# Optimization experiments

Hardware: AMD Instinct MI355X
Metric: run time of the kernel (lower is better)

## Reference

```python
import jax, jax.numpy as jnp
import numpy as np

EPS = 1e-3  # keras LayerNormalization default epsilon

def layernorm(x, gamma, beta):
    mu = jnp.mean(x, axis=-1, keepdims=True)
    var = jnp.var(x, axis=-1, keepdims=True)
    return (x - mu) * jax.lax.rsqrt(var + EPS) * gamma + beta

def setup_inputs() -> dict:
    key = jax.random.key(0)
    ks = jax.random.split(key, 20)
    B, N, T, Dimg, H = 512, 100, 14, 2048, 768
    s = lambda k, *sh: jax.random.normal(k, sh, dtype=jnp.float32) * 0.02
    return {
        "img_feat": jax.random.normal(ks[0], (B, N, Dimg), dtype=jnp.float32),
        "ques_feat": jax.random.normal(ks[1], (B, T, H), dtype=jnp.float32),
        "Wc": s(ks[2], Dimg, H), "bc": jnp.zeros((H,), jnp.float32),
        "Wq": s(ks[3], H, H),    "bq": jnp.zeros((H,), jnp.float32),
        "Wi": s(ks[4], Dimg, H), "bi": jnp.zeros((H,), jnp.float32),
        "wqa": s(ks[5], H, 1), "bqa": jnp.zeros((1,), jnp.float32),
        "wia": s(ks[6], H, 1), "bia": jnp.zeros((1,), jnp.float32),
        "g1": jnp.ones((N,), jnp.float32), "b1": jnp.zeros((N,), jnp.float32),
        "g2": jnp.ones((H,), jnp.float32), "b2": jnp.zeros((H,), jnp.float32),
        "g3": jnp.ones((T,), jnp.float32), "b3": jnp.zeros((T,), jnp.float32),
        "g4": jnp.ones((H,), jnp.float32), "b4": jnp.zeros((H,), jnp.float32),
        "g5": jnp.ones((N,), jnp.float32), "b5": jnp.zeros((N,), jnp.float32),
    }

def reference(img_feat, ques_feat, Wc, bc, Wq, bq, Wi, bi, wqa, bqa, wia, bia,
              g1, b1, g2, b2, g3, b3, g4, b4, g5, b5):
    # img_feat: [B,N,Dimg], ques_feat: [B,T,H]
    img_corr = img_feat @ Wc + bc                                   # [B,N,H]
    wm = jnp.einsum('bth,bnh->btn', ques_feat, img_corr)            # [B,T,N]
    wm = jax.nn.relu(layernorm(wm, g1, b1))
    ques_embed = ques_feat @ Wq + bq                                # [B,T,H]
    img_embed = img_feat @ Wi + bi                                  # [B,N,H]
    transform_img = jnp.einsum('btn,bnh->bth', wm, img_embed)       # [B,T,H]
    ques_atten_sum = jax.nn.relu(layernorm(transform_img + ques_embed, g2, b2))
    # dropout is identity at inference
    ques_atten = (ques_atten_sum @ wqa + bqa)[..., 0]               # [B,T]
    ques_atten = jax.nn.softmax(layernorm(ques_atten, g3, b3), axis=-1)
    transform_ques = jnp.einsum('btn,bth->bnh', wm, ques_embed)     # [B,N,H]
    img_atten_sum = jax.nn.relu(layernorm(transform_ques + img_embed, g4, b4))
    img_atten = (img_atten_sum @ wia + bia)[..., 0]                 # [B,N]
    img_atten = jax.nn.softmax(layernorm(img_atten, g5, b5), axis=-1)
    ques_atten_feat = jnp.einsum('bt,bth->bh', ques_atten, ques_feat)  # [B,H]
    img_atten_feat = jnp.einsum('bn,bnd->bd', img_atten, img_feat)     # [B,Dimg]
    return (img_atten_feat, ques_atten_feat)
```

## Files before the change

### kernel.cpp

```cpp
#include <hip/hip_runtime.h>

using f32x4     = __attribute__((ext_vector_type(4))) float;
using bf16x8    = __attribute__((ext_vector_type(8))) short;
using ushort8_t = __attribute__((ext_vector_type(8))) unsigned short;

__device__ __forceinline__ unsigned short f2bf(float f) {
    unsigned u = __builtin_bit_cast(unsigned, f);
    u += 0x7fffu + ((u >> 16) & 1u);
    return (unsigned short)(u >> 16);
}
__device__ __forceinline__ float bf2f(unsigned short h) {
    return __builtin_bit_cast(float, (unsigned)h << 16);
}

__device__ __forceinline__ float wave_sum(float v) {
#pragma unroll
    for (int off = 32; off > 0; off >>= 1) v += __shfl_xor(v, off, 64);
    return v;
}
__device__ __forceinline__ float wave_max(float v) {
#pragma unroll
    for (int off = 32; off > 0; off >>= 1) v = fmaxf(v, __shfl_xor(v, off, 64));
    return v;
}

#define GLP(p)  ((const __attribute__((address_space(1))) void*)(p))
#define LDSP(p) ((__attribute__((address_space(3))) void*)(p))

__global__ __launch_bounds__(256) void cvt2(
    const float* __restrict__ in0, unsigned short* __restrict__ out0, long n80,
    const float* __restrict__ in1, unsigned short* __restrict__ out1, long n81, int split)
{
    const float* in; unsigned short* out; long n8, i, stride;
    if ((int)blockIdx.x < split) {
        in = in0; out = out0; n8 = n80;
        i = (long)blockIdx.x * 256 + threadIdx.x; stride = (long)split * 256;
    } else {
        in = in1; out = out1; n8 = n81;
        i = (long)(blockIdx.x - split) * 256 + threadIdx.x;
        stride = (long)(gridDim.x - split) * 256;
    }
    for (; i < n8; i += stride) {
        const float4* p = (const float4*)(in + i * 8);
        float4 a = p[0], b = p[1];
        ushort8_t v;
        v[0] = f2bf(a.x); v[1] = f2bf(a.y); v[2] = f2bf(a.z); v[3] = f2bf(a.w);
        v[4] = f2bf(b.x); v[5] = f2bf(b.y); v[6] = f2bf(b.z); v[7] = f2bf(b.w);
        *(ushort8_t*)(out + i * 8) = v;
    }
}

__global__ __launch_bounds__(256) void pack_t(
    const float* __restrict__ S0, const float* __restrict__ S1, int nsplit,
    unsigned short* __restrict__ D, int K)
{
    __shared__ float t[64][65];
    const int k0 = blockIdx.x * 64, n0 = blockIdx.y * 64;
    const float* S = (n0 < nsplit) ? S0 : S1;
    const int nb = (n0 < nsplit) ? n0 : n0 - nsplit;
    const int c = threadIdx.x & 63, r4 = threadIdx.x >> 6;
#pragma unroll
    for (int it = 0; it < 16; ++it) {
        int r = it * 4 + r4;
        t[r][c] = S[(size_t)(k0 + r) * nsplit + nb + c];
    }
    __syncthreads();
#pragma unroll
    for (int it = 0; it < 16; ++it) {
        int rn = it * 4 + r4;
        D[(size_t)(n0 + rn) * K + k0 + c] = f2bf(t[c][rn]);
    }
}

__global__ __launch_bounds__(512, 1) void gemm8(
    const unsigned short* __restrict__ A1, const unsigned short* __restrict__ Bt1,
    const float* __restrict__ b1a, const float* __restrict__ b1b, int ns1,
    unsigned short* __restrict__ C1, int N1, int K1, int NTN1, int nblk1,
    const unsigned short* __restrict__ A2, const unsigned short* __restrict__ Bt2,
    const float* __restrict__ b2a, unsigned short* __restrict__ C2,
    int N2, int K2, int NTN2, int nblk2)
{
    __shared__ unsigned short LA[2][2][8192];
    __shared__ unsigned short LB[2][2][8192];
    const int tid = threadIdx.x, lane = tid & 63, wid = tid >> 6;

    int nwg = (int)gridDim.x, bid = (int)blockIdx.x;
    if ((nwg & 7) == 0) { int cpx = nwg >> 3; bid = (bid & 7) * cpx + (bid >> 3); }
    const unsigned short *A, *Bt; const float *bias0, *bias1;
    int nsplit, N, K, NTN; unsigned short* C;
    if (bid < nblk1) {
        A = A1; Bt = Bt1; bias0 = b1a; bias1 = b1b; nsplit = ns1;
        C = C1; N = N1; K = K1; NTN = NTN1;
    } else {
        bid -= nblk1;
        if (bid >= nblk2) return;
        A = A2; Bt = Bt2; bias0 = b2a; bias1 = b2a; nsplit = N2;
        C = C2; N = N2; K = K2; NTN = NTN2;
    }
    const int tn = bid % NTN, tm = bid / NTN;
    const size_t m0 = (size_t)tm * 256, n0 = (size_t)tn * 256;
    const int NT = K >> 6;
    const int NIT = NT >> 1;

    const int wr = wid >> 2, wc = wid & 3;
    const int hb = wc >> 1;
    const int fr = lane & 15, fs = lane >> 4;

    const int r0 = tid >> 3, s0 = ((tid & 7) - r0) & 7;
    const int r1 = r0 + 64,  s1 = ((tid & 7) - r1) & 7;
    const unsigned short* pA[2][2];
    const unsigned short* pB[2][2];
#pragma unroll
    for (int h = 0; h < 2; ++h) {
        pA[h][0] = A  + (m0 + h * 128 + r0) * K + s0 * 8;
        pA[h][1] = A  + (m0 + h * 128 + r1) * K + s1 * 8;
        pB[h][0] = Bt + (n0 + h * 128 + r0) * K + s0 * 8;
        pB[h][1] = Bt + (n0 + h * 128 + r1) * K + s1 * 8;
    }
    const int d0 = tid * 8, d1 = (tid + 512) * 8;

#define STG_A(h, t, B_) do { \
    __builtin_amdgcn_global_load_lds(GLP(pA[h][0] + (size_t)(t) * 64), LDSP(&LA[B_][h][d0]), 16, 0, 0); \
    __builtin_amdgcn_global_load_lds(GLP(pA[h][1] + (size_t)(t) * 64), LDSP(&LA[B_][h][d1]), 16, 0, 0); \
} while (0)
#define STG_B(h, t, B_) do { \
    __builtin_amdgcn_global_load_lds(GLP(pB[h][0] + (size_t)(t) * 64), LDSP(&LB[B_][h][d0]), 16, 0, 0); \
    __builtin_amdgcn_global_load_lds(GLP(pB[h][1] + (size_t)(t) * 64), LDSP(&LB[B_][h][d1]), 16, 0, 0); \
} while (0)

    int offA[2][4], offB[2][2];
#pragma unroll
    for (int mq = 0; mq < 2; ++mq)
#pragma unroll
        for (int mfl = 0; mfl < 4; ++mfl) {
            int r = mq * 64 + mfl * 16 + fr;
            offA[mq][mfl] = r * 64 + ((fs + r) & 7) * 8;
        }
#pragma unroll
    for (int nq = 0; nq < 2; ++nq)
#pragma unroll
        for (int nfl = 0; nfl < 2; ++nfl) {
            int r = (wc & 1) * 64 + nq * 32 + nfl * 16 + fr;
            offB[nq][nfl] = r * 64 + ((fs + r) & 7) * 8;
        }

#define LDA_SUB(B_, mq) do { \
    _Pragma("unroll") \
    for (int mfl = 0; mfl < 4; ++mfl) { \
        av[mfl][0] = *(const bf16x8*)&LA[B_][wr][offA[mq][mfl]]; \
        av[mfl][1] = *(const bf16x8*)&LA[B_][wr][offA[mq][mfl] ^ 32]; \
    } } while (0)
#define LDB_SUB(B_, nq, bv) do { \
    _Pragma("unroll") \
    for (int nfl = 0; nfl < 2; ++nfl) { \
        bv[nfl][0] = *(const bf16x8*)&LB[B_][hb][offB[nq][nfl]]; \
        bv[nfl][1] = *(const bf16x8*)&LB[B_][hb][offB[nq][nfl] ^ 32]; \
    } } while (0)
#define MMA_Q(mq, nq, bv) do { \
    _Pragma("unroll") \
    for (int ks = 0; ks < 2; ++ks) \
    _Pragma("unroll") \
    for (int mfl = 0; mfl < 4; ++mfl) \
    _Pragma("unroll") \
    for (int nfl = 0; nfl < 2; ++nfl) \
        acc[mq * 4 + mfl][nq * 2 + nfl] = __builtin_amdgcn_mfma_f32_16x16x32_bf16( \
            av[mfl][ks], bv[nfl][ks], acc[mq * 4 + mfl][nq * 2 + nfl], 0, 0, 0); \
    } while (0)
#define BAR  __builtin_amdgcn_s_barrier()
#define SCB  __builtin_amdgcn_sched_barrier(0)
#define LGKM0 do { asm volatile("s_waitcnt lgkmcnt(0)" ::: "memory"); SCB; } while (0)
#define PRIO1 __builtin_amdgcn_s_setprio(1)
#define PRIO0 __builtin_amdgcn_s_setprio(0)

    f32x4 acc[8][4];
#pragma unroll
    for (int i = 0; i < 8; ++i)
#pragma unroll
        for (int j = 0; j < 4; ++j) acc[i][j] = (f32x4){0.f, 0.f, 0.f, 0.f};

    STG_A(0, 0, 0); STG_A(1, 0, 0); STG_B(0, 0, 0); STG_B(1, 0, 0);
    STG_B(0, 1, 1); STG_B(1, 1, 1); STG_A(0, 1, 1);
    asm volatile("s_waitcnt vmcnt(6)" ::: "memory");
    SCB; BAR;

    for (int i = 0; i < NIT; ++i) {
        const int t0 = 2 * i, t1 = 2 * i + 1;
        const bool st = (i + 1 < NIT);
        bf16x8 av[4][2], bv0[2][2], bv1[2][2];

        LDA_SUB(0, 0); LDB_SUB(0, 0, bv0);
        STG_A(1, t1, 1);
        BAR; LGKM0;
        PRIO1; MMA_Q(0, 0, bv0); PRIO0;
        BAR;

        LDB_SUB(0, 1, bv1);
        BAR; LGKM0;
        PRIO1; MMA_Q(0, 1, bv1); PRIO0;
        BAR;

        LDA_SUB(0, 1);
        if (st) STG_B(0, t0 + 2, 0);
        BAR; LGKM0;
        PRIO1; MMA_Q(1, 1, bv1); PRIO0;
        BAR;

        if (st) { STG_B(1, t0 + 2, 0); STG_A(0, t0 + 2, 0); }
        BAR;
        PRIO1; MMA_Q(1, 0, bv0); PRIO0;
        if (st) asm volatile("s_waitcnt vmcnt(6)" ::: "memory");
        else    asm volatile("s_waitcnt vmcnt(0)" ::: "memory");
        SCB; BAR;

        LDA_SUB(1, 0); LDB_SUB(1, 0, bv0);
        if (st) STG_A(1, t0 + 2, 0);
        BAR; LGKM0;
        PRIO1; MMA_Q(0, 0, bv0); PRIO0;
        BAR;

        LDB_SUB(1, 1, bv1);
        BAR; LGKM0;
        PRIO1; MMA_Q(0, 1, bv1); PRIO0;
        BAR;

        LDA_SUB(1, 1);
        if (st) STG_B(0, t1 + 2, 1);
        BAR; LGKM0;
        PRIO1; MMA_Q(1, 1, bv1); PRIO0;
        BAR;

        if (st) { STG_B(1, t1 + 2, 1); STG_A(0, t1 + 2, 1); }
        BAR;
        PRIO1; MMA_Q(1, 0, bv0); PRIO0;
        if (st) asm volatile("s_waitcnt vmcnt(6)" ::: "memory");
        else    asm volatile("s_waitcnt vmcnt(0)" ::: "memory");
        SCB; BAR;
    }

#undef STG_A
#undef STG_B
#undef LDA_SUB
#undef LDB_SUB
#undef MMA_Q
#undef BAR
#undef SCB
#undef LGKM0
#undef PRIO1
#undef PRIO0

    const int wm = wr * 128, wn = wc * 64;
#pragma unroll
    for (int nf = 0; nf < 4; ++nf) {
        int col = (int)n0 + wn + nf * 16 + fr;
        float bs = (col < nsplit) ? bias0[col] : bias1[col - nsplit];
#pragma unroll
        for (int mf = 0; mf < 8; ++mf) {
            size_t rowb = m0 + wm + mf * 16 + fs * 4;
#pragma unroll
            for (int r = 0; r < 4; ++r)
                C[(rowb + r) * N + col] = f2bf(acc[mf][nf][r] + bs);
        }
    }
}

__global__ __launch_bounds__(256) void fused_kernel(
    const float* __restrict__ qf_g, const unsigned short* __restrict__ qbf,
    const unsigned short* __restrict__ qe_g, const unsigned short* __restrict__ imgCE,
    const unsigned short* __restrict__ imf_bf,
    const float* __restrict__ g1, const float* __restrict__ b1,
    const float* __restrict__ g2, const float* __restrict__ b2,
    const float* __restrict__ g3, const float* __restrict__ b3,
    const float* __restrict__ g4, const float* __restrict__ b4,
    const float* __restrict__ g5, const float* __restrict__ b5,
    const float* __restrict__ wqa, const float* __restrict__ bqa,
    const float* __restrict__ wia, const float* __restrict__ bia,
    float* __restrict__ out_i, float* __restrict__ out_q)
{
    const int b = blockIdx.x >> 1, role = blockIdx.x & 1;
    const int tid = threadIdx.x, lane = tid & 63, wid = tid >> 6;
    __shared__ unsigned short buf[14 * 768];
    __shared__ float wms[14 * 100];
    __shared__ float red[4][28];
    __shared__ float mu_s[14], rs_s[14], qa_s[14], qw_s[14];
    __shared__ float mu2_s[10], rs2_s[10];
    __shared__ float ia_s[100], iw_s[100];

    {
        const ushort8_t* src = (const ushort8_t*)(qbf + (size_t)b * 14 * 768);
        for (int i = tid; i < 14 * 768 / 8; i += 256) *(ushort8_t*)&buf[i * 8] = src[i];
    }
    __syncthreads();
    {
        float rcur[12], rnxt[12];
        {
            const unsigned short* row = imgCE + ((size_t)b * 100 + wid) * 1536;
#pragma unroll
            for (int j = 0; j < 12; ++j) rnxt[j] = bf2f(row[lane + 64 * j]);
        }
        for (int n = wid; n < 100; n += 4) {
#pragma unroll
            for (int j = 0; j < 12; ++j) rcur[j] = rnxt[j];
            if (n + 4 < 100) {
                const unsigned short* row = imgCE + ((size_t)b * 100 + n + 4) * 1536;
#pragma unroll
                for (int j = 0; j < 12; ++j) rnxt[j] = bf2f(row[lane + 64 * j]);
            }
            for (int t = 0; t < 14; ++t) {
                const unsigned short* q = buf + t * 768;
                float s = 0.f;
#pragma unroll
                for (int j = 0; j < 12; ++j) s = fmaf(rcur[j], bf2f(q[lane + 64 * j]), s);
                s = wave_sum(s);
                if (lane == 0) wms[t * 100 + n] = s;
            }
        }
    }
    __syncthreads();
    for (int t = wid; t < 14; t += 4) {
        float x0 = wms[t * 100 + lane];
        float x1 = (lane + 64 < 100) ? wms[t * 100 + lane + 64] : 0.f;
        float s = wave_sum(x0 + x1);
        float q = wave_sum(x0 * x0 + x1 * x1);
        float mu = s * (1.f / 100.f);
        float var = q * (1.f / 100.f) - mu * mu;
        float rs = rsqrtf(var + 1e-3f);
        {
            float v = (x0 - mu) * rs * g1[lane] + b1[lane];
            wms[t * 100 + lane] = v > 0.f ? v : 0.f;
        }
        if (lane + 64 < 100) {
            float v = (x1 - mu) * rs * g1[lane + 64] + b1[lane + 64];
            wms[t * 100 + lane + 64] = v > 0.f ? v : 0.f;
        }
    }
    {
        const ushort8_t* src = (const ushort8_t*)(qe_g + (size_t)b * 14 * 768);
        for (int i = tid; i < 14 * 768 / 8; i += 256) *(ushort8_t*)&buf[i * 8] = src[i];
    }
    __syncthreads();

    if (role == 0) {
        float a0[14], a1[14], a2[14];
#pragma unroll
        for (int t = 0; t < 14; ++t) { a0[t] = 0.f; a1[t] = 0.f; a2[t] = 0.f; }

        const unsigned short* ie_base = imgCE + (size_t)b * 100 * 1536 + 768;
        float e0n = bf2f(ie_base[tid]), e1n = bf2f(ie_base[tid + 256]), e2n = bf2f(ie_base[tid + 512]);
        for (int n = 0; n < 100; ++n) {
            float e0 = e0n, e1 = e1n, e2 = e2n;
            if (n < 99) {
                const unsigned short* ie = ie_base + (size_t)(n + 1) * 1536;
                e0n = bf2f(ie[tid]); e1n = bf2f(ie[tid + 256]); e2n = bf2f(ie[tid + 512]);
            }
#pragma unroll
            for (int t = 0; t < 14; ++t) {
                float w = wms[t * 100 + n];
                a0[t] = fmaf(w, e0, a0[t]); a1[t] = fmaf(w, e1, a1[t]); a2[t] = fmaf(w, e2, a2[t]);
            }
        }
#pragma unroll
        for (int t = 0; t < 14; ++t) {
            a0[t] += bf2f(buf[t * 768 + tid]);
            a1[t] += bf2f(buf[t * 768 + tid + 256]);
            a2[t] += bf2f(buf[t * 768 + tid + 512]);
        }
#pragma unroll
        for (int t = 0; t < 14; ++t) {
            float s = wave_sum(a0[t] + a1[t] + a2[t]);
            float q = wave_sum(a0[t] * a0[t] + a1[t] * a1[t] + a2[t] * a2[t]);
            if (lane == 0) { red[wid][t] = s; red[wid][14 + t] = q; }
        }
        __syncthreads();
        if (tid < 14) {
            float s = red[0][tid] + red[1][tid] + red[2][tid] + red[3][tid];
            float q = red[0][14 + tid] + red[1][14 + tid] + red[2][14 + tid] + red[3][14 + tid];
            float mu = s * (1.f / 768.f);
            float var = q * (1.f / 768.f) - mu * mu;
            mu_s[tid] = mu; rs_s[tid] = rsqrtf(var + 1e-3f);
        }
        __syncthreads();

        float ga = g2[tid], ba = b2[tid], gb = g2[tid + 256], bb = b2[tid + 256],
              gc = g2[tid + 512], bc_ = b2[tid + 512];
        float w0 = wqa[tid], w1 = wqa[tid + 256], w2 = wqa[tid + 512];
#pragma unroll
        for (int t = 0; t < 14; ++t) {
            float mu = mu_s[t], rs = rs_s[t];
            float v0 = fmaxf((a0[t] - mu) * rs * ga + ba, 0.f);
            float v1 = fmaxf((a1[t] - mu) * rs * gb + bb, 0.f);
            float v2 = fmaxf((a2[t] - mu) * rs * gc + bc_, 0.f);
            float p = wave_sum(v0 * w0 + v1 * w1 + v2 * w2);
            if (lane == 0) red[wid][t] = p;
        }
        __syncthreads();
        if (tid < 14) qa_s[tid] = red[0][tid] + red[1][tid] + red[2][tid] + red[3][tid] + bqa[0];
        __syncthreads();
        if (tid == 0) {
            float s = 0.f;
            for (int t = 0; t < 14; ++t) s += qa_s[t];
            float mu = s * (1.f / 14.f);
            float q = 0.f;
            for (int t = 0; t < 14; ++t) { float d = qa_s[t] - mu; q += d * d; }
            float rs = rsqrtf(q * (1.f / 14.f) + 1e-3f);
            float e[14], mx = -1e30f;
            for (int t = 0; t < 14; ++t) { e[t] = (qa_s[t] - mu) * rs * g3[t] + b3[t]; mx = fmaxf(mx, e[t]); }
            float se = 0.f;
            for (int t = 0; t < 14; ++t) { e[t] = expf(e[t] - mx); se += e[t]; }
            float inv = 1.f / se;
            for (int t = 0; t < 14; ++t) qw_s[t] = e[t] * inv;
        }
        __syncthreads();

        const float* qf = qf_g + (size_t)b * 14 * 768;
#pragma unroll
        for (int c = 0; c < 3; ++c) {
            int h = tid + c * 256;
            float o = 0.f;
#pragma unroll
            for (int t = 0; t < 14; ++t) o = fmaf(qw_s[t], qf[t * 768 + h], o);
            out_q[(size_t)b * 768 + h] = o;
        }
    } else {
        float g4a = g4[tid], b4a = b4[tid], g4b = g4[tid + 256], b4b = b4[tid + 256],
              g4c = g4[tid + 512], b4c = b4[tid + 512];
        float wa = wia[tid], wb = wia[tid + 256], wc_ = wia[tid + 512];

        for (int g = 0; g < 10; ++g) {
            float ge0[10], ge1[10], ge2[10];
#pragma unroll
            for (int i = 0; i < 10; ++i) {
                const unsigned short* ie = imgCE + ((size_t)b * 100 + g * 10 + i) * 1536 + 768;
                ge0[i] = bf2f(ie[tid]); ge1[i] = bf2f(ie[tid + 256]); ge2[i] = bf2f(ie[tid + 512]);
            }
            float t0[10], t1[10], t2[10];
#pragma unroll
            for (int i = 0; i < 10; ++i) { t0[i] = 0.f; t1[i] = 0.f; t2[i] = 0.f; }
#pragma unroll
            for (int t = 0; t < 14; ++t) {
                float q0 = bf2f(buf[t * 768 + tid]), q1 = bf2f(buf[t * 768 + tid + 256]),
                      q2 = bf2f(buf[t * 768 + tid + 512]);
#pragma unroll
                for (int i = 0; i < 10; ++i) {
                    float w = wms[t * 100 + g * 10 + i];
                    t0[i] = fmaf(w, q0, t0[i]); t1[i] = fmaf(w, q1, t1[i]); t2[i] = fmaf(w, q2, t2[i]);
                }
            }
#pragma unroll
            for (int i = 0; i < 10; ++i) {
                t0[i] += ge0[i]; t1[i] += ge1[i]; t2[i] += ge2[i];
                float s = wave_sum(t0[i] + t1[i] + t2[i]);
                float q = wave_sum(t0[i] * t0[i] + t1[i] * t1[i] + t2[i] * t2[i]);
                if (lane == 0) { red[wid][i] = s; red[wid][10 + i] = q; }
            }
            __syncthreads();
            if (tid < 10) {
                float s = red[0][tid] + red[1][tid] + red[2][tid] + red[3][tid];
                float q = red[0][10 + tid] + red[1][10 + tid] + red[2][10 + tid] + red[3][10 + tid];
                float mu = s * (1.f / 768.f);
                float var = q * (1.f / 768.f) - mu * mu;
                mu2_s[tid] = mu; rs2_s[tid] = rsqrtf(var + 1e-3f);
            }
            __syncthreads();
#pragma unroll
            for (int i = 0; i < 10; ++i) {
                float mu = mu2_s[i], rs = rs2_s[i];
                float v0 = fmaxf((t0[i] - mu) * rs * g4a + b4a, 0.f);
                float v1 = fmaxf((t1[i] - mu) * rs * g4b + b4b, 0.f);
                float v2 = fmaxf((t2[i] - mu) * rs * g4c + b4c, 0.f);
                float p = wave_sum(v0 * wa + v1 * wb + v2 * wc_);
                if (lane == 0) red[wid][i] = p;
            }
            __syncthreads();
            if (tid < 10) ia_s[g * 10 + tid] = red[0][tid] + red[1][tid] + red[2][tid] + red[3][tid] + bia[0];
            __syncthreads();
        }

        if (wid == 0) {
            float x0 = ia_s[lane];
            float x1 = (lane + 64 < 100) ? ia_s[lane + 64] : 0.f;
            float s = wave_sum(x0 + x1);
            float q = wave_sum(x0 * x0 + x1 * x1);
            float mu = s * 0.01f;
            float var = q * 0.01f - mu * mu;
            float rs = rsqrtf(var + 1e-3f);
            float v0 = (x0 - mu) * rs * g5[lane] + b5[lane];
            float v1 = (lane + 64 < 100) ? (x1 - mu) * rs * g5[lane + 64] + b5[lane + 64] : -1e30f;
            float mx = wave_max(fmaxf(v0, v1));
            float e0 = expf(v0 - mx);
            float e1 = (lane + 64 < 100) ? expf(v1 - mx) : 0.f;
            float se = wave_sum(e0 + e1);
            float inv = 1.f / se;
            iw_s[lane] = e0 * inv;
            if (lane + 64 < 100) iw_s[lane + 64] = e1 * inv;
        }
        __syncthreads();

        const unsigned short* imf = imf_bf + (size_t)b * 100 * 2048;
        float acc8[8];
#pragma unroll
        for (int j = 0; j < 8; ++j) acc8[j] = 0.f;
        for (int n = 0; n < 100; ++n) {
            ushort8_t v = *(const ushort8_t*)(imf + (size_t)n * 2048 + tid * 8);
            float w = iw_s[n];
#pragma unroll
            for (int j = 0; j < 8; ++j) acc8[j] = fmaf(w, bf2f(v[j]), acc8[j]);
        }
        float4* dst = (float4*)(out_i + (size_t)b * 2048);
        float4 oA = {acc8[0], acc8[1], acc8[2], acc8[3]};
        float4 oB = {acc8[4], acc8[5], acc8[6], acc8[7]};
        dst[tid * 2] = oA; dst[tid * 2 + 1] = oB;
    }
}

extern "C" void kernel_launch(void* const* d_in, const int* in_sizes, int n_in,
                              void* d_out, int out_size, void* d_ws, size_t ws_size,
                              hipStream_t stream)
{
    const float* img_feat = (const float*)d_in[0];
    const float* ques_feat = (const float*)d_in[1];
    const float* Wc = (const float*)d_in[2];
    const float* bc = (const float*)d_in[3];
    const float* Wq = (const float*)d_in[4];
    const float* bq = (const float*)d_in[5];
    const float* Wi = (const float*)d_in[6];
    const float* bi = (const float*)d_in[7];
    const float* wqa = (const float*)d_in[8];
    const float* bqa = (const float*)d_in[9];
    const float* wia = (const float*)d_in[10];
    const float* bia = (const float*)d_in[11];
    const float* g1 = (const float*)d_in[12]; const float* b1 = (const float*)d_in[13];
    const float* g2 = (const float*)d_in[14]; const float* b2 = (const float*)d_in[15];
    const float* g3 = (const float*)d_in[16]; const float* b3 = (const float*)d_in[17];
    const float* g4 = (const float*)d_in[18]; const float* b4 = (const float*)d_in[19];
    const float* g5 = (const float*)d_in[20]; const float* b5 = (const float*)d_in[21];

    const size_t SZ_WP   = 1536u * 2048u * 2u;
    const size_t SZ_WQT  = 768u * 768u * 2u;
    const size_t SZ_IMG  = 51200ull * 1536u * 2u;
    const size_t SZ_QE   = 7168u * 768u * 4u;
    const size_t SZ_WM   = 512u * 1400u * 4u;
    const size_t SZ_ABF  = 51200ull * 2048u * 2u;
    const size_t SZ_QBF  = 7168u * 768u * 2u;

    const size_t OFF_WP  = 0;
    const size_t OFF_WQT = OFF_WP + SZ_WP;
    const size_t OFF_IMG = OFF_WQT + SZ_WQT;
    const size_t OFF_QE  = OFF_IMG + SZ_IMG;
    const size_t OFF_WM  = OFF_QE + SZ_QE;
    const size_t OFF_ABF = OFF_WM + SZ_WM;
    const size_t OFF_QBF = OFF_ABF + SZ_ABF;
    const size_t NEED    = OFF_QBF + SZ_QBF;
    if (ws_size < NEED) return;

    char* ws = (char*)d_ws;
    unsigned short* Wp    = (unsigned short*)(ws + OFF_WP);
    unsigned short* Wqt   = (unsigned short*)(ws + OFF_WQT);
    unsigned short* imgCE = (unsigned short*)(ws + OFF_IMG);
    unsigned short* qe    = (unsigned short*)(ws + OFF_QE);
    unsigned short* Abf   = (unsigned short*)(ws + OFF_ABF);
    unsigned short* Qbf   = (unsigned short*)(ws + OFF_QBF);

    float* out_img = (float*)d_out;
    float* out_q   = (float*)d_out + 512 * 2048;

    hipLaunchKernelGGL(pack_t, dim3(32, 24), dim3(256), 0, stream, Wc, Wi, 768, Wp, 2048);
    hipLaunchKernelGGL(pack_t, dim3(12, 12), dim3(256), 0, stream, Wq, Wq, 768, Wqt, 768);
    hipLaunchKernelGGL(cvt2, dim3(2304), dim3(256), 0, stream,
                       img_feat, Abf, (long)(51200ull * 2048u / 8u),
                       ques_feat, Qbf, (long)(7168u * 768u / 8u), 2048);

    hipLaunchKernelGGL(gemm8, dim3(1288), dim3(512), 0, stream,
                       Abf, Wp, bc, bi, 768, imgCE, 1536, 2048, 6, 1200,
                       Qbf, Wqt, bq, qe, 768, 768, 3, 84);

    hipLaunchKernelGGL(fused_kernel, dim3(1024), dim3(256), 0, stream,
                       ques_feat, Qbf, qe, imgCE, Abf,
                       g1, b1, g2, b2, g3, b3, g4, b4, g5, b5,
                       wqa, bqa, wia, bia, out_img, out_q);
}
```

Baseline: 907.6 us.

## Split merged GEMM launch into two launches and merge fused-kernel roles per batch

The single grouped GEMM launch covering both the image and question projections becomes two separate launches of a templated GEMM, which removes the per-block problem dispatch. The fused kernel now runs one block per batch that does both the question-attention and image-attention roles in sequence, instead of two blocks per batch each recomputing the shared prologue (wm layernorm and loads). This removes the duplicated prologue work but halves the grid to 512 blocks and serialises the two roles inside each block. It also adds a launch and loses overlap between the small question GEMM and the large image GEMM.

```diff
diff --git a/kernel.cpp b/kernel.cpp
--- a/kernel.cpp
+++ b/kernel.cpp
@@ -72,13 +72,11 @@
     }
 }
 
+template <int OUTBF>
 __global__ __launch_bounds__(512, 1) void gemm8(
-    const unsigned short* __restrict__ A1, const unsigned short* __restrict__ Bt1,
-    const float* __restrict__ b1a, const float* __restrict__ b1b, int ns1,
-    unsigned short* __restrict__ C1, int N1, int K1, int NTN1, int nblk1,
-    const unsigned short* __restrict__ A2, const unsigned short* __restrict__ Bt2,
-    const float* __restrict__ b2a, unsigned short* __restrict__ C2,
-    int N2, int K2, int NTN2, int nblk2)
+    const unsigned short* __restrict__ A, const unsigned short* __restrict__ Bt,
+    const float* __restrict__ bias0, const float* __restrict__ bias1, int nsplit,
+    void* __restrict__ Cv, int N, int K, int NTN)
 {
     __shared__ unsigned short LA[2][2][8192];
     __shared__ unsigned short LB[2][2][8192];
@@ -86,17 +84,6 @@
 
     int nwg = (int)gridDim.x, bid = (int)blockIdx.x;
     if ((nwg & 7) == 0) { int cpx = nwg >> 3; bid = (bid & 7) * cpx + (bid >> 3); }
-    const unsigned short *A, *Bt; const float *bias0, *bias1;
-    int nsplit, N, K, NTN; unsigned short* C;
-    if (bid < nblk1) {
-        A = A1; Bt = Bt1; bias0 = b1a; bias1 = b1b; nsplit = ns1;
-        C = C1; N = N1; K = K1; NTN = NTN1;
-    } else {
-        bid -= nblk1;
-        if (bid >= nblk2) return;
-        A = A2; Bt = Bt2; bias0 = b2a; bias1 = b2a; nsplit = N2;
-        C = C2; N = N2; K = K2; NTN = NTN2;
-    }
     const int tn = bid % NTN, tm = bid / NTN;
     const size_t m0 = (size_t)tm * 256, n0 = (size_t)tn * 256;
     const int NT = K >> 6;
@@ -257,8 +244,11 @@
         for (int mf = 0; mf < 8; ++mf) {
             size_t rowb = m0 + wm + mf * 16 + fs * 4;
 #pragma unroll
-            for (int r = 0; r < 4; ++r)
-                C[(rowb + r) * N + col] = f2bf(acc[mf][nf][r] + bs);
+            for (int r = 0; r < 4; ++r) {
+                float v = acc[mf][nf][r] + bs;
+                if (OUTBF) ((unsigned short*)Cv)[(rowb + r) * N + col] = f2bf(v);
+                else       ((float*)Cv)[(rowb + r) * N + col] = v;
+            }
         }
     }
 }
@@ -276,7 +266,7 @@
     const float* __restrict__ wia, const float* __restrict__ bia,
     float* __restrict__ out_i, float* __restrict__ out_q)
 {
-    const int b = blockIdx.x >> 1, role = blockIdx.x & 1;
+    const int b = blockIdx.x;
     const int tid = threadIdx.x, lane = tid & 63, wid = tid >> 6;
     __shared__ unsigned short buf[14 * 768];
     __shared__ float wms[14 * 100];
@@ -339,7 +329,7 @@
     }
     __syncthreads();
 
-    if (role == 0) {
+    {
         float a0[14], a1[14], a2[14];
 #pragma unroll
         for (int t = 0; t < 14; ++t) { a0[t] = 0.f; a1[t] = 0.f; a2[t] = 0.f; }
@@ -420,7 +410,10 @@
             for (int t = 0; t < 14; ++t) o = fmaf(qw_s[t], qf[t * 768 + h], o);
             out_q[(size_t)b * 768 + h] = o;
         }
-    } else {
+    }
+    __syncthreads();
+
+    {
         float g4a = g4[tid], b4a = b4[tid], g4b = g4[tid + 256], b4b = b4[tid + 256],
               g4c = g4[tid + 512], b4c = b4[tid + 512];
         float wa = wia[tid], wb = wia[tid + 256], wc_ = wia[tid + 512];
@@ -569,11 +562,12 @@
                        img_feat, Abf, (long)(51200ull * 2048u / 8u),
                        ques_feat, Qbf, (long)(7168u * 768u / 8u), 2048);
 
-    hipLaunchKernelGGL(gemm8, dim3(1288), dim3(512), 0, stream,
-                       Abf, Wp, bc, bi, 768, imgCE, 1536, 2048, 6, 1200,
-                       Qbf, Wqt, bq, qe, 768, 768, 3, 84);
-
-    hipLaunchKernelGGL(fused_kernel, dim3(1024), dim3(256), 0, stream,
+    hipLaunchKernelGGL(HIP_KERNEL_NAME(gemm8<1>), dim3(1200), dim3(512), 0, stream,
+                       Abf, Wp, bc, bi, 768, (void*)imgCE, 1536, 2048, 6);
+    hipLaunchKernelGGL(HIP_KERNEL_NAME(gemm8<1>), dim3(84), dim3(512), 0, stream,
+                       Qbf, Wqt, bq, bq, 768, (void*)qe, 768, 768, 3);
+
+    hipLaunchKernelGGL(fused_kernel, dim3(512), dim3(256), 0, stream,
                        ques_feat, Qbf, qe, imgCE, Abf,
                        g1, b1, g2, b2, g3, b3, g4, b4, g5, b5,
                        wqa, bqa, wia, bia, out_img, out_q);
```

Measured after the change: 766.3 us. -15.6%, faster.
